# Kernel optimization log

Measured on AMD Instinct MI355X. Metric: run time of the kernel, lower is better.

Reference implementation:

```python
import jax, jax.numpy as jnp
import numpy as np
from jax.scipy.special import logsumexp

EPS = 0.1
MAX_ITER = 50
THRESH = 0.1


def setup_inputs() -> dict:
    key = jax.random.key(0)
    k1, k2, k3 = jax.random.split(key, 3)
    B, N, M = 64, 1024, 1024
    pred = jax.random.uniform(k1, (B, N), dtype=jnp.float32)
    pred = pred / pred.sum(-1, keepdims=True)
    target = jax.random.uniform(k2, (B, M), dtype=jnp.float32)
    target = target / target.sum(-1, keepdims=True)
    C = jax.random.uniform(k3, (B, N, M), dtype=jnp.float32)
    return {"pred": pred, "target": target, "C": C}


def _sinkhorn(pred, target, C):
    # Modified cost for log-domain updates: M_ij = (-C_ij + u_i + v_j) / eps
    def Mmat(u, v):
        return (-C + u[..., :, None] + v[..., None, :]) / EPS

    log_mu = jnp.log(pred + 1e-8)   # [B, N]
    log_nu = jnp.log(target + 1e-8)  # [B, M]

    def body(carry, _):
        u, v, done = carry
        u1 = u
        u_new = EPS * (log_mu - logsumexp(Mmat(u, v), axis=-1)) + u
        v_new = EPS * (log_nu - logsumexp(Mmat(u_new, v), axis=-2)) + v
        err = jnp.abs(u_new - u1).sum(-1).mean()
        # emulate the torch early-break: freeze u, v once converged
        u = jnp.where(done, u, u_new)
        v = jnp.where(done, v, v_new)
        done = done | (err < THRESH)
        return (u, v, done), None

    u0 = jnp.zeros_like(pred)
    v0 = jnp.zeros_like(target)
    (u, v, _), _ = jax.lax.scan(body, (u0, v0, jnp.array(False)), None, length=MAX_ITER)

    pi = jnp.exp(Mmat(u, v))                 # transport plan [B, N, M]
    dist = jnp.sum(pi * C, axis=(-2, -1))    # [B]
    dist = dist.mean()                       # reduction='mean'
    return dist, pi


def reference(pred, target, C):
    return _sinkhorn(pred, target, C)
```

## Files before the change

kernel.cpp:

```cpp
#include <hip/hip_runtime.h>
#include <math.h>

#define Bsz 64
#define Nn  1024
#define Mm  1024
#define NB   1024
#define NSUB 32
#define SUBN (NB/NSUB)

constexpr float EPS_F    = 0.1f;
constexpr float INV_EPS  = 10.0f;
constexpr int   MAX_IT   = 50;
constexpr float THRESH_F = 0.1f;

#define U_OFF    0
#define V_OFF    (Bsz*Nn)
#define LMU_OFF  (2*Bsz*Nn)
#define LNU_OFF  (3*Bsz*Nn)
#define ERR_OFF  (4*Bsz*Nn)
#define BSUM_OFF (4*Bsz*Nn + 64)
#define BAR_OFF  (4*Bsz*Nn + 128)
#define BAR_ROOT (NSUB*16)
#define BAR_GEN  (NSUB*16 + 16)
#define BAR_FLAG (NSUB*16 + 32)
#define ZERO_N   (128 + NSUB*16 + 48)

__device__ __forceinline__ float wave_max(float x) {
    #pragma unroll
    for (int off = 32; off > 0; off >>= 1) x = fmaxf(x, __shfl_xor(x, off));
    return x;
}
__device__ __forceinline__ float wave_sum(float x) {
    #pragma unroll
    for (int off = 32; off > 0; off >>= 1) x += __shfl_xor(x, off);
    return x;
}

__device__ __forceinline__ void gbar(unsigned* bar) {
    __threadfence();
    __syncthreads();
    if (threadIdx.x == 0) {
        unsigned* gen  = bar + BAR_GEN;
        unsigned* root = bar + BAR_ROOT;
        unsigned g = __hip_atomic_load(gen, __ATOMIC_RELAXED, __HIP_MEMORY_SCOPE_AGENT);
        bool flip = false;
        unsigned a = __hip_atomic_fetch_add(bar + (blockIdx.x & (NSUB-1))*16, 1u,
                                            __ATOMIC_ACQ_REL, __HIP_MEMORY_SCOPE_AGENT);
        if (a == SUBN - 1) {
            unsigned r = __hip_atomic_fetch_add(root, 1u,
                                                __ATOMIC_ACQ_REL, __HIP_MEMORY_SCOPE_AGENT);
            if (r == NSUB - 1) {
                #pragma unroll
                for (int k = 0; k < NSUB; ++k)
                    __hip_atomic_store(bar + k*16, 0u, __ATOMIC_RELAXED,
                                       __HIP_MEMORY_SCOPE_AGENT);
                __hip_atomic_store(root, 0u, __ATOMIC_RELAXED, __HIP_MEMORY_SCOPE_AGENT);
                __hip_atomic_fetch_add(gen, 1u, __ATOMIC_RELEASE, __HIP_MEMORY_SCOPE_AGENT);
                flip = true;
            }
        }
        if (!flip) {
            while (__hip_atomic_load(gen, __ATOMIC_RELAXED, __HIP_MEMORY_SCOPE_AGENT) == g)
                __builtin_amdgcn_s_sleep(2);
        }
        __threadfence();
    }
    __syncthreads();
}

__global__ void ot_zero(float* __restrict__ ws) {
    for (int i = threadIdx.x; i < ZERO_N; i += 256) ws[ERR_OFF + i] = 0.f;
}

__global__ __launch_bounds__(256, 4) void ot_all(
        const float* __restrict__ pred, const float* __restrict__ target,
        const float* __restrict__ C, float* __restrict__ ws,
        float* __restrict__ out)
{
    const int tid  = threadIdx.x;
    const int bid  = blockIdx.x;
    const int lane = tid & 63;
    const int wv   = tid >> 6;
    unsigned* bar   = (unsigned*)(ws + BAR_OFF);
    unsigned* flagp = bar + BAR_FLAG;

    __shared__ float s_u[Nn];
    __shared__ float s_m[4][64];
    __shared__ float s_s[4][64];
    __shared__ float s_err[4];

    {
        int g = (bid << 8) + tid;
        if (g < Bsz*Nn) {
            ws[U_OFF + g]   = 0.f;
            ws[LMU_OFF + g] = logf(pred[g] + 1e-8f);
            ws[V_OFF + g]   = 0.f;
            ws[LNU_OFF + g] = logf(target[g] + 1e-8f);
        }
    }
    gbar(bar);

    const int w    = (bid << 2) + wv;
    const int row0 = w << 4;
    const int bR   = row0 >> 10;
    const int bC   = bid >> 4;
    const int jt   = bid & 15;
    const int q    = tid >> 6;
    const int j    = (jt << 6) + lane;

    for (int t = 0; t < MAX_IT; ++t) {
        if (__hip_atomic_load(flagp, __ATOMIC_RELAXED, __HIP_MEMORY_SCOPE_AGENT) != 0u)
            break;

        {
            const float4* vp = (const float4*)(ws + V_OFF + ((size_t)bR << 10));
            float4 v4[4];
            #pragma unroll
            for (int k = 0; k < 4; ++k) v4[k] = vp[lane + (k << 6)];

            const float4* cr = (const float4*)(C + ((size_t)row0 << 10));
            float4 c4[4], n4[4];
            #pragma unroll
            for (int k = 0; k < 4; ++k) c4[k] = cr[lane + (k << 6)];

            float errw = 0.f;
            #pragma unroll 1
            for (int r = 0; r < 16; ++r) {
                if (r + 1 < 16) {
                    const float4* nx = cr + ((size_t)(r + 1) << 8);
                    #pragma unroll
                    for (int k = 0; k < 4; ++k) n4[k] = nx[lane + (k << 6)];
                }
                float xs[16];
                #pragma unroll
                for (int k = 0; k < 4; ++k) {
                    xs[4*k+0] = (v4[k].x - c4[k].x) * INV_EPS;
                    xs[4*k+1] = (v4[k].y - c4[k].y) * INV_EPS;
                    xs[4*k+2] = (v4[k].z - c4[k].z) * INV_EPS;
                    xs[4*k+3] = (v4[k].w - c4[k].w) * INV_EPS;
                }
                float m = xs[0];
                #pragma unroll
                for (int k = 1; k < 16; ++k) m = fmaxf(m, xs[k]);
                m = wave_max(m);
                float s = 0.f;
                #pragma unroll
                for (int k = 0; k < 16; ++k) s += __expf(xs[k] - m);
                s = wave_sum(s);
                float lse = m + logf(s);

                int row = row0 + r;
                float unew = EPS_F * (ws[LMU_OFF + row] - lse);
                errw += fabsf(unew - ws[U_OFF + row]);
                if (lane == 0) ws[U_OFF + row] = unew;

                if (r + 1 < 16) {
                    #pragma unroll
                    for (int k = 0; k < 4; ++k) c4[k] = n4[k];
                }
            }
            if (lane == 0) s_err[wv] = errw;
            __syncthreads();
            if (tid == 0)
                atomicAdd(ws + ERR_OFF + t, s_err[0]+s_err[1]+s_err[2]+s_err[3]);
        }
        gbar(bar);

        {
            #pragma unroll
            for (int k = 0; k < 4; ++k)
                s_u[tid + (k << 8)] = ws[U_OFF + (bC << 10) + tid + (k << 8)];
            __syncthreads();

            const float* cp = C + (((size_t)bC << 10) + (q << 8)) * Mm + j;
            const float* us = &s_u[q << 8];
            float m = -INFINITY, s = 0.f;
            #pragma unroll 8
            for (int i = 0; i < 256; ++i) {
                float c  = cp[(size_t)i * Mm];
                float x  = (us[i] - c) * INV_EPS;
                float mn = fmaxf(m, x);
                s = s * __expf(m - mn) + __expf(x - mn);
                m = mn;
            }
            s_m[q][lane] = m;
            s_s[q][lane] = s;
            __syncthreads();
            if (q == 0) {
                float m0=s_m[0][lane], m1=s_m[1][lane], m2=s_m[2][lane], m3=s_m[3][lane];
                float gm = fmaxf(fmaxf(m0,m1), fmaxf(m2,m3));
                float gs = s_s[0][lane]*__expf(m0-gm) + s_s[1][lane]*__expf(m1-gm)
                         + s_s[2][lane]*__expf(m2-gm) + s_s[3][lane]*__expf(m3-gm);
                float lse = gm + logf(gs);
                ws[V_OFF + (bC << 10) + j] =
                    EPS_F * (ws[LNU_OFF + (bC << 10) + j] - lse);
            }
            if (bid == 0 && tid == 0) {
                float e = ws[ERR_OFF + t];
                if (e * (1.0f/64.0f) < THRESH_F)
                    __hip_atomic_store(flagp, 1u, __ATOMIC_RELAXED,
                                       __HIP_MEMORY_SCOPE_AGENT);
            }
        }
        gbar(bar);
    }

    {
        const float4* vp = (const float4*)(ws + V_OFF + ((size_t)bR << 10));
        float4 v4[4];
        #pragma unroll
        for (int k = 0; k < 4; ++k) v4[k] = vp[lane + (k << 6)];
        const float4* cr = (const float4*)(C + ((size_t)row0 << 10));
        float dot = 0.f;
        #pragma unroll 1
        for (int r = 0; r < 16; ++r) {
            int row = row0 + r;
            float u_i = ws[U_OFF + row];
            const float4* cx = cr + ((size_t)r << 8);
            float4 c4[4];
            #pragma unroll
            for (int k = 0; k < 4; ++k) c4[k] = cx[lane + (k << 6)];
            float4* po = (float4*)(out + 1 + ((size_t)row << 10));
            #pragma unroll
            for (int k = 0; k < 4; ++k) {
                float4 p;
                p.x = __expf((u_i + v4[k].x - c4[k].x) * INV_EPS);
                p.y = __expf((u_i + v4[k].y - c4[k].y) * INV_EPS);
                p.z = __expf((u_i + v4[k].z - c4[k].z) * INV_EPS);
                p.w = __expf((u_i + v4[k].w - c4[k].w) * INV_EPS);
                po[lane + (k << 6)] = p;
                dot += p.x*c4[k].x + p.y*c4[k].y + p.z*c4[k].z + p.w*c4[k].w;
            }
        }
        dot = wave_sum(dot);
        if (lane == 0) atomicAdd(ws + BSUM_OFF + bR, dot);
    }
    gbar(bar);
    if (bid == 0 && tid < 64) {
        float x = wave_sum(ws[BSUM_OFF + tid]);
        if (tid == 0) out[0] = x * (1.0f/64.0f);
    }
}

extern "C" void kernel_launch(void* const* d_in, const int* in_sizes, int n_in,
                              void* d_out, int out_size, void* d_ws, size_t ws_size,
                              hipStream_t stream)
{
    const float* pred   = (const float*)d_in[0];
    const float* target = (const float*)d_in[1];
    const float* C      = (const float*)d_in[2];
    float* ws  = (float*)d_ws;
    float* out = (float*)d_out;

    ot_zero<<<1, 256, 0, stream>>>(ws);
    ot_all<<<NB, 256, 0, stream>>>(pred, target, C, ws, out);
}
```

Measured before the change: 1.859 ms.

## Fuse column log-sum-exp into row pass to read C once per iteration

```diff
diff --git a/kernel.cpp b/kernel.cpp
--- a/kernel.cpp
+++ b/kernel.cpp
@@ -17,19 +17,14 @@
 #define V_OFF    (Bsz*Nn)
 #define LMU_OFF  (2*Bsz*Nn)
 #define LNU_OFF  (3*Bsz*Nn)
-#define ERR_OFF  (4*Bsz*Nn)
-#define BSUM_OFF (4*Bsz*Nn + 64)
-#define BAR_OFF  (4*Bsz*Nn + 128)
+#define ERRB_OFF (4*Bsz*Nn)
+#define DOT_OFF  (4*Bsz*Nn + 1024)
+#define BAR_OFF  (4*Bsz*Nn + 1024 + 4096)
 #define BAR_ROOT (NSUB*16)
 #define BAR_GEN  (NSUB*16 + 16)
 #define BAR_FLAG (NSUB*16 + 32)
-#define ZERO_N   (128 + NSUB*16 + 48)
-
-__device__ __forceinline__ float wave_max(float x) {
-    #pragma unroll
-    for (int off = 32; off > 0; off >>= 1) x = fmaxf(x, __shfl_xor(x, off));
-    return x;
-}
+#define BAR_N    (NSUB*16 + 48)
+
 __device__ __forceinline__ float wave_sum(float x) {
     #pragma unroll
     for (int off = 32; off > 0; off >>= 1) x += __shfl_xor(x, off);
@@ -69,7 +64,8 @@
 }
 
 __global__ void ot_zero(float* __restrict__ ws) {
-    for (int i = threadIdx.x; i < ZERO_N; i += 256) ws[ERR_OFF + i] = 0.f;
+    unsigned* bar = (unsigned*)(ws + BAR_OFF);
+    for (int i = threadIdx.x; i < BAR_N; i += 256) bar[i] = 0u;
 }
 
 __global__ __launch_bounds__(256, 4) void ot_all(
@@ -83,11 +79,12 @@
     const int wv   = tid >> 6;
     unsigned* bar   = (unsigned*)(ws + BAR_OFF);
     unsigned* flagp = bar + BAR_FLAG;
-
-    __shared__ float s_u[Nn];
+    float* part = out + 1;
+
+    __shared__ float s_part[4][Nn];
     __shared__ float s_m[4][64];
-    __shared__ float s_s[4][64];
     __shared__ float s_err[4];
+    __shared__ int   s_flag;
 
     {
         int g = (bid << 8) + tid;
@@ -109,21 +106,32 @@
     const int j    = (jt << 6) + lane;
 
     for (int t = 0; t < MAX_IT; ++t) {
-        if (__hip_atomic_load(flagp, __ATOMIC_RELAXED, __HIP_MEMORY_SCOPE_AGENT) != 0u)
-            break;
+        if (tid == 0)
+            s_flag = (__hip_atomic_load(flagp, __ATOMIC_RELAXED,
+                                        __HIP_MEMORY_SCOPE_AGENT) != 0u);
+        __syncthreads();
+        if (s_flag) break;
 
         {
             const float4* vp = (const float4*)(ws + V_OFF + ((size_t)bR << 10));
-            float4 v4[4];
-            #pragma unroll
-            for (int k = 0; k < 4; ++k) v4[k] = vp[lane + (k << 6)];
+            float vv[16];
+            #pragma unroll
+            for (int k = 0; k < 4; ++k) {
+                float4 v4 = vp[lane + (k << 6)];
+                vv[4*k+0] = v4.x * INV_EPS; vv[4*k+1] = v4.y * INV_EPS;
+                vv[4*k+2] = v4.z * INV_EPS; vv[4*k+3] = v4.w * INV_EPS;
+            }
 
             const float4* cr = (const float4*)(C + ((size_t)row0 << 10));
             float4 c4[4], n4[4];
             #pragma unroll
             for (int k = 0; k < 4; ++k) c4[k] = cr[lane + (k << 6)];
 
+            float scol[16];
+            #pragma unroll
+            for (int k = 0; k < 16; ++k) scol[k] = 0.f;
             float errw = 0.f;
+
             #pragma unroll 1
             for (int r = 0; r < 16; ++r) {
                 if (r + 1 < 16) {
@@ -131,75 +139,86 @@
                     #pragma unroll
                     for (int k = 0; k < 4; ++k) n4[k] = nx[lane + (k << 6)];
                 }
-                float xs[16];
+                float ce[16];
                 #pragma unroll
                 for (int k = 0; k < 4; ++k) {
-                    xs[4*k+0] = (v4[k].x - c4[k].x) * INV_EPS;
-                    xs[4*k+1] = (v4[k].y - c4[k].y) * INV_EPS;
-                    xs[4*k+2] = (v4[k].z - c4[k].z) * INV_EPS;
-                    xs[4*k+3] = (v4[k].w - c4[k].w) * INV_EPS;
-                }
-                float m = xs[0];
-                #pragma unroll
-                for (int k = 1; k < 16; ++k) m = fmaxf(m, xs[k]);
-                m = wave_max(m);
-                float s = 0.f;
-                #pragma unroll
-                for (int k = 0; k < 16; ++k) s += __expf(xs[k] - m);
-                s = wave_sum(s);
-                float lse = m + logf(s);
+                    ce[4*k+0] = c4[k].x; ce[4*k+1] = c4[k].y;
+                    ce[4*k+2] = c4[k].z; ce[4*k+3] = c4[k].w;
+                }
+                float er[16];
+                #pragma unroll
+                for (int k = 0; k < 16; ++k)
+                    er[k] = __expf(__builtin_fmaf(ce[k], -INV_EPS, vv[k]));
+                float srow = 0.f;
+                #pragma unroll
+                for (int k = 0; k < 16; ++k) srow += er[k];
+                srow = wave_sum(srow);
+                float lse = logf(srow);
 
                 int row = row0 + r;
-                float unew = EPS_F * (ws[LMU_OFF + row] - lse);
+                float lmu  = ws[LMU_OFF + row];
+                float unew = EPS_F * (lmu - lse);
                 errw += fabsf(unew - ws[U_OFF + row]);
                 if (lane == 0) ws[U_OFF + row] = unew;
+
+                float uu = lmu - lse;
+                #pragma unroll
+                for (int k = 0; k < 16; ++k)
+                    scol[k] += __expf(__builtin_fmaf(ce[k], -INV_EPS, uu));
 
                 if (r + 1 < 16) {
                     #pragma unroll
                     for (int k = 0; k < 4; ++k) c4[k] = n4[k];
                 }
             }
+
+            #pragma unroll
+            for (int k = 0; k < 4; ++k) {
+                float4 p = {scol[4*k+0], scol[4*k+1], scol[4*k+2], scol[4*k+3]};
+                *((float4*)&s_part[wv][(k << 8) + (lane << 2)]) = p;
+            }
             if (lane == 0) s_err[wv] = errw;
             __syncthreads();
+            {
+                int j4 = tid << 2;
+                float4 a = *((float4*)&s_part[0][j4]);
+                float4 b = *((float4*)&s_part[1][j4]);
+                float4 c = *((float4*)&s_part[2][j4]);
+                float4 d = *((float4*)&s_part[3][j4]);
+                float4 sm = {a.x+b.x+c.x+d.x, a.y+b.y+c.y+d.y,
+                             a.z+b.z+c.z+d.z, a.w+b.w+c.w+d.w};
+                ((float4*)(part + ((size_t)bid << 10)))[tid] = sm;
+            }
             if (tid == 0)
-                atomicAdd(ws + ERR_OFF + t, s_err[0]+s_err[1]+s_err[2]+s_err[3]);
+                ws[ERRB_OFF + bid] = s_err[0]+s_err[1]+s_err[2]+s_err[3];
         }
         gbar(bar);
 
         {
-            #pragma unroll
-            for (int k = 0; k < 4; ++k)
-                s_u[tid + (k << 8)] = ws[U_OFF + (bC << 10) + tid + (k << 8)];
-            __syncthreads();
-
-            const float* cp = C + (((size_t)bC << 10) + (q << 8)) * Mm + j;
-            const float* us = &s_u[q << 8];
-            float m = -INFINITY, s = 0.f;
-            #pragma unroll 8
-            for (int i = 0; i < 256; ++i) {
-                float c  = cp[(size_t)i * Mm];
-                float x  = (us[i] - c) * INV_EPS;
-                float mn = fmaxf(m, x);
-                s = s * __expf(m - mn) + __expf(x - mn);
-                m = mn;
-            }
-            s_m[q][lane] = m;
-            s_s[q][lane] = s;
+            float s = 0.f;
+            #pragma unroll
+            for (int r = 0; r < 4; ++r) {
+                int p = (bC << 4) + (q << 2) + r;
+                s += part[((size_t)p << 10) + j];
+            }
+            s_m[q][lane] = s;
             __syncthreads();
             if (q == 0) {
-                float m0=s_m[0][lane], m1=s_m[1][lane], m2=s_m[2][lane], m3=s_m[3][lane];
-                float gm = fmaxf(fmaxf(m0,m1), fmaxf(m2,m3));
-                float gs = s_s[0][lane]*__expf(m0-gm) + s_s[1][lane]*__expf(m1-gm)
-                         + s_s[2][lane]*__expf(m2-gm) + s_s[3][lane]*__expf(m3-gm);
-                float lse = gm + logf(gs);
+                float stot = s_m[0][lane] + s_m[1][lane] + s_m[2][lane] + s_m[3][lane];
                 ws[V_OFF + (bC << 10) + j] =
-                    EPS_F * (ws[LNU_OFF + (bC << 10) + j] - lse);
-            }
-            if (bid == 0 && tid == 0) {
-                float e = ws[ERR_OFF + t];
-                if (e * (1.0f/64.0f) < THRESH_F)
-                    __hip_atomic_store(flagp, 1u, __ATOMIC_RELAXED,
-                                       __HIP_MEMORY_SCOPE_AGENT);
+                    EPS_F * (ws[LNU_OFF + (bC << 10) + j] - logf(stot));
+            }
+            if (bid == 0) {
+                float4 e4 = ((const float4*)(ws + ERRB_OFF))[tid];
+                float e = wave_sum(e4.x + e4.y + e4.z + e4.w);
+                if (lane == 0) s_err[wv] = e;
+                __syncthreads();
+                if (tid == 0) {
+                    float tot = s_err[0]+s_err[1]+s_err[2]+s_err[3];
+                    if (tot * (1.0f/64.0f) < THRESH_F)
+                        __hip_atomic_store(flagp, 1u, __ATOMIC_RELAXED,
+                                           __HIP_MEMORY_SCOPE_AGENT);
+                }
             }
         }
         gbar(bar);
@@ -233,12 +252,18 @@
             }
         }
         dot = wave_sum(dot);
-        if (lane == 0) atomicAdd(ws + BSUM_OFF + bR, dot);
+        if (lane == 0) ws[DOT_OFF + w] = dot;
     }
     gbar(bar);
-    if (bid == 0 && tid < 64) {
-        float x = wave_sum(ws[BSUM_OFF + tid]);
-        if (tid == 0) out[0] = x * (1.0f/64.0f);
+    if (bid == 0) {
+        float s = 0.f;
+        #pragma unroll
+        for (int k = 0; k < 16; ++k) s += ws[DOT_OFF + (k << 8) + tid];
+        s = wave_sum(s);
+        if (lane == 0) s_err[wv] = s;
+        __syncthreads();
+        if (tid == 0)
+            out[0] = (s_err[0]+s_err[1]+s_err[2]+s_err[3]) * (1.0f/64.0f);
     }
 }
 
```

Result: faster. 1.778 ms (-4.4%).
